# Optimization experiments

Hardware: AMD Instinct MI355X
Metric: run time of the kernel (lower is better)

Reference implementation:

```python
import jax, jax.numpy as jnp
import numpy as np

NUM_HEADS = 16


def setup_inputs() -> dict:
    key = jax.random.key(0)
    ks = jax.random.split(key, 8)
    B_, N, C = 2048, 64, 512
    nW = 64
    return {
        "x": jax.random.normal(ks[0], (B_, N, C), dtype=jnp.float32),
        "pe": jax.random.normal(ks[1], (1, N, C), dtype=jnp.float32),
        "rpe": jax.random.normal(ks[2], (NUM_HEADS, N, N), dtype=jnp.float32),
        "mask": jax.random.normal(ks[3], (nW, N, N), dtype=jnp.float32),
        "qkv_w": jax.random.normal(ks[4], (3 * C, C), dtype=jnp.float32) * 0.02,
        "qkv_b": jax.random.normal(ks[5], (3 * C,), dtype=jnp.float32) * 0.02,
        "proj_w": jax.random.normal(ks[6], (C, C), dtype=jnp.float32) * 0.02,
        "proj_b": jax.random.normal(ks[7], (C,), dtype=jnp.float32) * 0.02,
    }


def reference(x, pe, rpe, mask, qkv_w, qkv_b, proj_w, proj_b):
    B_, N, C = x.shape
    H = NUM_HEADS
    hd = C // H
    scale = hd ** -0.5
    xp = x + pe  # (B_, N, C)
    qkv = xp @ qkv_w.T + qkv_b  # (B_, N, 3C)
    qkv = qkv.reshape(B_, N, 3, H, hd).transpose(2, 0, 3, 1, 4)  # (3, B_, H, N, hd)
    q, k, v = qkv[0], qkv[1], qkv[2]
    attn = jnp.einsum("bhnd,bhmd->bhnm", q * scale, k)  # (B_, H, N, N)
    attn = attn + rpe[None]  # broadcast rpe over batch
    nW = mask.shape[0]
    attn = attn.reshape(B_ // nW, nW, H, N, N) + mask[None, :, None]
    attn = attn.reshape(B_, H, N, N)
    attn = jax.nn.softmax(attn, axis=-1)
    out = jnp.einsum("bhnm,bhmd->bhnd", attn, v)  # (B_, H, N, hd)
    out = out.transpose(0, 2, 1, 3).reshape(B_, N, C)
    return out @ proj_w.T + proj_b
```

## Files before the change

kernel.cpp:

```cpp
#include <hip/hip_runtime.h>
#include <hip/hip_bf16.h>
#include <cstdint>

typedef __bf16 bf16;
typedef __bf16 bf16x8_t __attribute__((ext_vector_type(8)));
typedef __bf16 bf16x4_t __attribute__((ext_vector_type(4)));
typedef float  f32x4_t  __attribute__((ext_vector_type(4)));

#define MFMA16(a, b, c) __builtin_amdgcn_mfma_f32_16x16x32_bf16((a), (b), (c), 0, 0, 0)

__global__ void k_wprep(const float* __restrict__ wq, const float* __restrict__ wp,
                        bf16* __restrict__ wqb, bf16* __restrict__ wpb) {
    int t = blockIdx.x * 256 + threadIdx.x;
    int stride = gridDim.x * 256;
    for (int i = t; i < 196608; i += stride) {
        float4 v = ((const float4*)wq)[i];
        bf16x4_t o; o[0]=(bf16)v.x; o[1]=(bf16)v.y; o[2]=(bf16)v.z; o[3]=(bf16)v.w;
        ((bf16x4_t*)wqb)[i] = o;
    }
    for (int i = t; i < 65536; i += stride) {
        float4 v = ((const float4*)wp)[i];
        bf16x4_t o; o[0]=(bf16)v.x; o[1]=(bf16)v.y; o[2]=(bf16)v.z; o[3]=(bf16)v.w;
        ((bf16x4_t*)wpb)[i] = o;
    }
}

__global__ __launch_bounds__(256) void k_qkv_attn(
    const float* __restrict__ x,
    const float* __restrict__ pe,
    const float* __restrict__ rpe,
    const float* __restrict__ mask,
    const float* __restrict__ qkv_b,
    const bf16*  __restrict__ wq,
    bf16* __restrict__ ao)
{
    __shared__ bf16 Ws[96 * 72];
    __shared__ bf16 qs[64 * 40];
    __shared__ bf16 ks[64 * 40];
    __shared__ bf16 vts[32 * 72];
    __shared__ bf16 ps[64 * 72];

    const int b    = blockIdx.x;
    const int tid  = threadIdx.x;
    const int lane = tid & 63;
    const int wave = tid >> 6;
    const int lr   = lane & 15;
    const int lg   = lane >> 4;
    const int row0 = wave * 16;
    const int wi   = b & 63;

    bf16x8_t a[16];
    {
        const float* xr = x  + ((size_t)(b * 64 + row0 + lr)) * 512;
        const float* pr = pe + (size_t)(row0 + lr) * 512;
#pragma unroll
        for (int kc = 0; kc < 16; ++kc) {
            int k = kc * 32 + lg * 8;
            float4 x0 = *(const float4*)(xr + k);
            float4 x1 = *(const float4*)(xr + k + 4);
            float4 p0 = *(const float4*)(pr + k);
            float4 p1 = *(const float4*)(pr + k + 4);
            bf16x8_t v;
            v[0]=(bf16)(x0.x+p0.x); v[1]=(bf16)(x0.y+p0.y);
            v[2]=(bf16)(x0.z+p0.z); v[3]=(bf16)(x0.w+p0.w);
            v[4]=(bf16)(x1.x+p1.x); v[5]=(bf16)(x1.y+p1.y);
            v[6]=(bf16)(x1.z+p1.z); v[7]=(bf16)(x1.w+p1.w);
            a[kc] = v;
        }
    }

    const float SCALE = 0.17677669529663687f;

    for (int h = 0; h < 16; ++h) {
        f32x4_t acc[6] = {};
#pragma unroll
        for (int kt = 0; kt < 8; ++kt) {
            bf16x8_t wst[3];
#pragma unroll
            for (int j = 0; j < 3; ++j) {
                int c = tid + 256 * j;
                int rr = c >> 3, i8 = (c & 7) * 8;
                int n = ((rr >> 5) << 9) + (h << 5) + (rr & 31);
                wst[j] = *(const bf16x8_t*)(wq + (size_t)n * 512 + kt * 64 + i8);
            }
            __syncthreads();
#pragma unroll
            for (int j = 0; j < 3; ++j) {
                int c = tid + 256 * j;
                int rr = c >> 3, i8 = (c & 7) * 8;
                *(bf16x8_t*)&Ws[rr * 72 + i8] = wst[j];
            }
            __syncthreads();
#pragma unroll
            for (int k2 = 0; k2 < 2; ++k2) {
                const int kc = kt * 2 + k2;
#pragma unroll
                for (int j = 0; j < 6; ++j) {
                    bf16x8_t bfrag = *(const bf16x8_t*)&Ws[(j * 16 + lr) * 72 + k2 * 32 + lg * 8];
                    acc[j] = MFMA16(a[kc], bfrag, acc[j]);
                }
            }
        }

#pragma unroll
        for (int j = 0; j < 6; ++j) {
            int which = j >> 1;
            int colh  = (j & 1) * 16 + lr;
            float bj = qkv_b[which * 512 + h * 32 + colh];
#pragma unroll
            for (int r = 0; r < 4; ++r) {
                int row = row0 + lg * 4 + r;
                float val = acc[j][r] + bj;
                if (which == 0)      qs[row * 40 + colh] = (bf16)val;
                else if (which == 1) ks[row * 40 + colh] = (bf16)val;
                else                 vts[colh * 72 + row] = (bf16)val;
            }
        }
        __syncthreads();

        bf16x8_t aq = *(const bf16x8_t*)&qs[(row0 + lr) * 40 + lg * 8];
        f32x4_t s[4];
        f32x4_t zero = {};
#pragma unroll
        for (int j = 0; j < 4; ++j) {
            bf16x8_t bk = *(const bf16x8_t*)&ks[(j * 16 + lr) * 40 + lg * 8];
            s[j] = MFMA16(aq, bk, zero);
        }

        const float* rp = rpe  + ((size_t)h)  * 4096;
        const float* mp = mask + ((size_t)wi) * 4096;
        float pv_[4][4];
        float mx[4] = {-1e30f, -1e30f, -1e30f, -1e30f};
#pragma unroll
        for (int j = 0; j < 4; ++j) {
            int col = j * 16 + lr;
#pragma unroll
            for (int r = 0; r < 4; ++r) {
                int row = row0 + lg * 4 + r;
                float t = s[j][r] * SCALE + rp[row * 64 + col] + mp[row * 64 + col];
                pv_[j][r] = t;
                mx[r] = fmaxf(mx[r], t);
            }
        }
#pragma unroll
        for (int r = 0; r < 4; ++r) {
            float m = mx[r];
            m = fmaxf(m, __shfl_xor(m, 1));
            m = fmaxf(m, __shfl_xor(m, 2));
            m = fmaxf(m, __shfl_xor(m, 4));
            m = fmaxf(m, __shfl_xor(m, 8));
            mx[r] = m;
        }
        float sm[4] = {0.f, 0.f, 0.f, 0.f};
#pragma unroll
        for (int j = 0; j < 4; ++j)
#pragma unroll
            for (int r = 0; r < 4; ++r) {
                float e = __expf(pv_[j][r] - mx[r]);
                pv_[j][r] = e;
                sm[r] += e;
            }
#pragma unroll
        for (int r = 0; r < 4; ++r) {
            float ssum = sm[r];
            ssum += __shfl_xor(ssum, 1);
            ssum += __shfl_xor(ssum, 2);
            ssum += __shfl_xor(ssum, 4);
            ssum += __shfl_xor(ssum, 8);
            sm[r] = 1.0f / ssum;
        }
#pragma unroll
        for (int j = 0; j < 4; ++j)
#pragma unroll
            for (int r = 0; r < 4; ++r)
                ps[(row0 + lg * 4 + r) * 72 + j * 16 + lr] = (bf16)pv_[j][r];

        f32x4_t o[2] = {};
#pragma unroll
        for (int kh = 0; kh < 2; ++kh) {
            bf16x8_t pa = *(const bf16x8_t*)&ps[(row0 + lr) * 72 + kh * 32 + lg * 8];
#pragma unroll
            for (int jd = 0; jd < 2; ++jd) {
                bf16x8_t bv = *(const bf16x8_t*)&vts[(jd * 16 + lr) * 72 + kh * 32 + lg * 8];
                o[jd] = MFMA16(pa, bv, o[jd]);
            }
        }
#pragma unroll
        for (int jd = 0; jd < 2; ++jd)
#pragma unroll
            for (int r = 0; r < 4; ++r) {
                int row = row0 + lg * 4 + r;
                ao[((size_t)(b * 64 + row)) * 512 + h * 32 + jd * 16 + lr] =
                    (bf16)(o[jd][r] * sm[r]);
            }
    }
}

__global__ __launch_bounds__(256) void k_proj(
    const bf16* __restrict__ A, const bf16* __restrict__ Bw,
    const float* __restrict__ bias, float* __restrict__ C)
{
    __shared__ bf16 As[128 * 40];
    __shared__ bf16 Bs[128 * 40];

    const int tid  = threadIdx.x;
    const int lane = tid & 63;
    const int wave = tid >> 6;
    const int lr = lane & 15, lg = lane >> 4;
    const int wr = wave >> 1, wc = wave & 1;
    const int mb = blockIdx.x >> 2, nb = blockIdx.x & 3;
    const size_t m0 = (size_t)mb * 128;
    const int n0 = nb * 128;

    f32x4_t acc[4][4] = {};

    for (int kt = 0; kt < 16; ++kt) {
        const int k0 = kt * 32;
        bf16x8_t va[2], vb[2];
#pragma unroll
        for (int j = 0; j < 2; ++j) {
            int c = tid + 256 * j;
            int row = c >> 2, i8 = (c & 3) * 8;
            va[j] = *(const bf16x8_t*)(A  + (m0 + row) * 512 + k0 + i8);
            vb[j] = *(const bf16x8_t*)(Bw + (size_t)(n0 + row) * 512 + k0 + i8);
        }
        __syncthreads();
#pragma unroll
        for (int j = 0; j < 2; ++j) {
            int c = tid + 256 * j;
            int row = c >> 2, i8 = (c & 3) * 8;
            *(bf16x8_t*)&As[row * 40 + i8] = va[j];
            *(bf16x8_t*)&Bs[row * 40 + i8] = vb[j];
        }
        __syncthreads();

        bf16x8_t af[4], bfr[4];
#pragma unroll
        for (int i = 0; i < 4; ++i)
            af[i] = *(const bf16x8_t*)&As[(wr * 64 + i * 16 + lr) * 40 + lg * 8];
#pragma unroll
        for (int j = 0; j < 4; ++j)
            bfr[j] = *(const bf16x8_t*)&Bs[(wc * 64 + j * 16 + lr) * 40 + lg * 8];
#pragma unroll
        for (int i = 0; i < 4; ++i)
#pragma unroll
            for (int j = 0; j < 4; ++j)
                acc[i][j] = MFMA16(af[i], bfr[j], acc[i][j]);
    }

    float bj[4];
#pragma unroll
    for (int j = 0; j < 4; ++j) bj[j] = bias[n0 + wc * 64 + j * 16 + lr];
#pragma unroll
    for (int i = 0; i < 4; ++i) {
#pragma unroll
        for (int j = 0; j < 4; ++j) {
            int col = n0 + wc * 64 + j * 16 + lr;
#pragma unroll
            for (int r = 0; r < 4; ++r) {
                size_t row = m0 + wr * 64 + i * 16 + lg * 4 + r;
                C[row * 512 + col] = acc[i][j][r] + bj[j];
            }
        }
    }
}

extern "C" void kernel_launch(void* const* d_in, const int* in_sizes, int n_in,
                              void* d_out, int out_size, void* d_ws, size_t ws_size,
                              hipStream_t stream) {
    (void)in_sizes; (void)n_in; (void)out_size; (void)ws_size;
    const float* x      = (const float*)d_in[0];
    const float* pe     = (const float*)d_in[1];
    const float* rpe    = (const float*)d_in[2];
    const float* mask   = (const float*)d_in[3];
    const float* qkv_w  = (const float*)d_in[4];
    const float* qkv_b  = (const float*)d_in[5];
    const float* proj_w = (const float*)d_in[6];
    const float* proj_b = (const float*)d_in[7];
    float* out = (float*)d_out;

    char* ws = (char*)d_ws;
    bf16* wqkvb  = (bf16*)ws;
    bf16* wprojb = (bf16*)(ws + 1572864);
    bf16* ao     = (bf16*)(ws + 2097152);

    k_wprep<<<256, 256, 0, stream>>>(qkv_w, proj_w, wqkvb, wprojb);
    k_qkv_attn<<<2048, 256, 0, stream>>>(x, pe, rpe, mask, qkv_b, wqkvb, ao);
    k_proj<<<4096, 256, 0, stream>>>(ao, wprojb, proj_b, out);
}
```

Measured before the change: 679.0 us.

## Share QKV weight tiles across two windows per block via direct-to-LDS loads

The fused QKV+attention kernel now runs 512-thread blocks that each process two windows, so every weight tile staged in shared memory is reused by twice as many waves. Weight staging uses global_load_lds with an XOR-swizzled layout and 128-wide K tiles, which removes the register round trip and halves the number of K iterations. The rpe+mask loads are issued before the QK MFMAs so their latency can overlap, and k_proj gets a remapped block order aimed at cache locality. The costs are more LDS per block, a launch bound that may constrain registers, and a __syncthreads now shared by 8 waves.

```diff
diff --git a/kernel.cpp b/kernel.cpp
--- a/kernel.cpp
+++ b/kernel.cpp
@@ -8,6 +8,13 @@
 typedef float  f32x4_t  __attribute__((ext_vector_type(4)));
 
 #define MFMA16(a, b, c) __builtin_amdgcn_mfma_f32_16x16x32_bf16((a), (b), (c), 0, 0, 0)
+
+__device__ __forceinline__ void gload_lds16(const bf16* g, bf16* l) {
+    __builtin_amdgcn_global_load_lds(
+        (const __attribute__((address_space(1))) void*)g,
+        (__attribute__((address_space(3))) void*)l,
+        16, 0, 0);
+}
 
 __global__ void k_wprep(const float* __restrict__ wq, const float* __restrict__ wp,
                         bf16* __restrict__ wqb, bf16* __restrict__ wpb) {
@@ -25,7 +32,7 @@
     }
 }
 
-__global__ __launch_bounds__(256) void k_qkv_attn(
+__global__ __launch_bounds__(512, 4) void k_qkv_attn(
     const float* __restrict__ x,
     const float* __restrict__ pe,
     const float* __restrict__ rpe,
@@ -34,24 +41,25 @@
     const bf16*  __restrict__ wq,
     bf16* __restrict__ ao)
 {
-    __shared__ bf16 Ws[96 * 72];
-    __shared__ bf16 qs[64 * 40];
-    __shared__ bf16 ks[64 * 40];
-    __shared__ bf16 vts[32 * 72];
-    __shared__ bf16 ps[64 * 72];
-
-    const int b    = blockIdx.x;
+    __shared__ bf16 Ws[96 * 128];
+    __shared__ bf16 qs[2][64 * 40];
+    __shared__ bf16 ks[2][64 * 40];
+    __shared__ bf16 vts[2][32 * 72];
+    __shared__ bf16 ps[2][64 * 72];
+
     const int tid  = threadIdx.x;
     const int lane = tid & 63;
     const int wave = tid >> 6;
+    const int win  = wave >> 2;
     const int lr   = lane & 15;
     const int lg   = lane >> 4;
-    const int row0 = wave * 16;
-    const int wi   = b & 63;
+    const int row0 = (wave & 3) * 16;
+    const int b2   = blockIdx.x * 2 + win;
+    const int wi   = b2 & 63;
 
     bf16x8_t a[16];
     {
-        const float* xr = x  + ((size_t)(b * 64 + row0 + lr)) * 512;
+        const float* xr = x  + ((size_t)(b2 * 64 + row0 + lr)) * 512;
         const float* pr = pe + (size_t)(row0 + lr) * 512;
 #pragma unroll
         for (int kc = 0; kc < 16; ++kc) {
@@ -74,32 +82,31 @@
     for (int h = 0; h < 16; ++h) {
         f32x4_t acc[6] = {};
 #pragma unroll
-        for (int kt = 0; kt < 8; ++kt) {
-            bf16x8_t wst[3];
-#pragma unroll
-            for (int j = 0; j < 3; ++j) {
-                int c = tid + 256 * j;
-                int rr = c >> 3, i8 = (c & 7) * 8;
-                int n = ((rr >> 5) << 9) + (h << 5) + (rr & 31);
-                wst[j] = *(const bf16x8_t*)(wq + (size_t)n * 512 + kt * 64 + i8);
+        for (int kt = 0; kt < 4; ++kt) {
+#pragma unroll
+            for (int ii = 0; ii < 3; ++ii) {
+                int instr = wave * 3 + ii;
+                int r  = instr * 4 + (lane >> 4);
+                int s  = lane & 15;
+                int gp = (s & 8) | ((s & 7) ^ (r & 7));
+                int R  = ((r >> 5) << 9) + (h << 5) + (r & 31);
+                gload_lds16(wq + (size_t)R * 512 + kt * 128 + gp * 8,
+                            &Ws[instr * 512]);
             }
             __syncthreads();
 #pragma unroll
-            for (int j = 0; j < 3; ++j) {
-                int c = tid + 256 * j;
-                int rr = c >> 3, i8 = (c & 7) * 8;
-                *(bf16x8_t*)&Ws[rr * 72 + i8] = wst[j];
-            }
-            __syncthreads();
-#pragma unroll
-            for (int k2 = 0; k2 < 2; ++k2) {
-                const int kc = kt * 2 + k2;
+            for (int k2 = 0; k2 < 4; ++k2) {
+                const int kc = kt * 4 + k2;
 #pragma unroll
                 for (int j = 0; j < 6; ++j) {
-                    bf16x8_t bfrag = *(const bf16x8_t*)&Ws[(j * 16 + lr) * 72 + k2 * 32 + lg * 8];
+                    int row  = j * 16 + lr;
+                    int p    = k2 * 4 + lg;
+                    int phys = (p & 8) | ((p & 7) ^ (row & 7));
+                    bf16x8_t bfrag = *(const bf16x8_t*)&Ws[row * 128 + phys * 8];
                     acc[j] = MFMA16(a[kc], bfrag, acc[j]);
                 }
             }
+            __syncthreads();
         }
 
 #pragma unroll
@@ -111,37 +118,44 @@
             for (int r = 0; r < 4; ++r) {
                 int row = row0 + lg * 4 + r;
                 float val = acc[j][r] + bj;
-                if (which == 0)      qs[row * 40 + colh] = (bf16)val;
-                else if (which == 1) ks[row * 40 + colh] = (bf16)val;
-                else                 vts[colh * 72 + row] = (bf16)val;
+                if (which == 0)      qs[win][row * 40 + colh] = (bf16)val;
+                else if (which == 1) ks[win][row * 40 + colh] = (bf16)val;
+                else                 vts[win][colh * 72 + row] = (bf16)val;
             }
         }
         __syncthreads();
 
-        bf16x8_t aq = *(const bf16x8_t*)&qs[(row0 + lr) * 40 + lg * 8];
+        const float* rp = rpe  + ((size_t)h)  * 4096;
+        const float* mp = mask + ((size_t)wi) * 4096;
+        float rm[4][4];
+#pragma unroll
+        for (int j = 0; j < 4; ++j) {
+            int col = j * 16 + lr;
+#pragma unroll
+            for (int r = 0; r < 4; ++r) {
+                int row = row0 + lg * 4 + r;
+                rm[j][r] = rp[row * 64 + col] + mp[row * 64 + col];
+            }
+        }
+
+        bf16x8_t aq = *(const bf16x8_t*)&qs[win][(row0 + lr) * 40 + lg * 8];
         f32x4_t s[4];
         f32x4_t zero = {};
 #pragma unroll
         for (int j = 0; j < 4; ++j) {
-            bf16x8_t bk = *(const bf16x8_t*)&ks[(j * 16 + lr) * 40 + lg * 8];
+            bf16x8_t bk = *(const bf16x8_t*)&ks[win][(j * 16 + lr) * 40 + lg * 8];
             s[j] = MFMA16(aq, bk, zero);
         }
 
-        const float* rp = rpe  + ((size_t)h)  * 4096;
-        const float* mp = mask + ((size_t)wi) * 4096;
-        float pv_[4][4];
         float mx[4] = {-1e30f, -1e30f, -1e30f, -1e30f};
 #pragma unroll
-        for (int j = 0; j < 4; ++j) {
-            int col = j * 16 + lr;
-#pragma unroll
-            for (int r = 0; r < 4; ++r) {
-                int row = row0 + lg * 4 + r;
-                float t = s[j][r] * SCALE + rp[row * 64 + col] + mp[row * 64 + col];
-                pv_[j][r] = t;
+        for (int j = 0; j < 4; ++j)
+#pragma unroll
+            for (int r = 0; r < 4; ++r) {
+                float t = s[j][r] * SCALE + rm[j][r];
+                s[j][r] = t;
                 mx[r] = fmaxf(mx[r], t);
             }
-        }
 #pragma unroll
         for (int r = 0; r < 4; ++r) {
             float m = mx[r];
@@ -156,8 +170,8 @@
         for (int j = 0; j < 4; ++j)
 #pragma unroll
             for (int r = 0; r < 4; ++r) {
-                float e = __expf(pv_[j][r] - mx[r]);
-                pv_[j][r] = e;
+                float e = __expf(s[j][r] - mx[r]);
+                s[j][r] = e;
                 sm[r] += e;
             }
 #pragma unroll
@@ -173,15 +187,15 @@
         for (int j = 0; j < 4; ++j)
 #pragma unroll
             for (int r = 0; r < 4; ++r)
-                ps[(row0 + lg * 4 + r) * 72 + j * 16 + lr] = (bf16)pv_[j][r];
+                ps[win][(row0 + lg * 4 + r) * 72 + j * 16 + lr] = (bf16)s[j][r];
 
         f32x4_t o[2] = {};
 #pragma unroll
         for (int kh = 0; kh < 2; ++kh) {
-            bf16x8_t pa = *(const bf16x8_t*)&ps[(row0 + lr) * 72 + kh * 32 + lg * 8];
+            bf16x8_t pa = *(const bf16x8_t*)&ps[win][(row0 + lr) * 72 + kh * 32 + lg * 8];
 #pragma unroll
             for (int jd = 0; jd < 2; ++jd) {
-                bf16x8_t bv = *(const bf16x8_t*)&vts[(jd * 16 + lr) * 72 + kh * 32 + lg * 8];
+                bf16x8_t bv = *(const bf16x8_t*)&vts[win][(jd * 16 + lr) * 72 + kh * 32 + lg * 8];
                 o[jd] = MFMA16(pa, bv, o[jd]);
             }
         }
@@ -190,7 +204,7 @@
 #pragma unroll
             for (int r = 0; r < 4; ++r) {
                 int row = row0 + lg * 4 + r;
-                ao[((size_t)(b * 64 + row)) * 512 + h * 32 + jd * 16 + lr] =
+                ao[((size_t)(b2 * 64 + row)) * 512 + h * 32 + jd * 16 + lr] =
                     (bf16)(o[jd][r] * sm[r]);
             }
     }
@@ -208,7 +222,9 @@
     const int wave = tid >> 6;
     const int lr = lane & 15, lg = lane >> 4;
     const int wr = wave >> 1, wc = wave & 1;
-    const int mb = blockIdx.x >> 2, nb = blockIdx.x & 3;
+    const int bid = blockIdx.x;
+    const int wg  = (bid & 7) * 512 + (bid >> 3);
+    const int mb = wg >> 2, nb = wg & 3;
     const size_t m0 = (size_t)mb * 128;
     const int n0 = nb * 128;
 
@@ -285,6 +301,6 @@
     bf16* ao     = (bf16*)(ws + 2097152);
 
     k_wprep<<<256, 256, 0, stream>>>(qkv_w, proj_w, wqkvb, wprojb);
-    k_qkv_attn<<<2048, 256, 0, stream>>>(x, pe, rpe, mask, qkv_b, wqkvb, ao);
+    k_qkv_attn<<<1024, 512, 0, stream>>>(x, pe, rpe, mask, qkv_b, wqkvb, ao);
     k_proj<<<4096, 256, 0, stream>>>(ao, wprojb, proj_b, out);
 }
```

Measured after the change: 762.1 us. +12.2%, slower.
